# Kernel tuning notes

Hardware: AMD Instinct MI355X
Metric: run time of the kernel (lower is better)

## Reference

```python
import jax, jax.numpy as jnp
import numpy as np

B, S, H = 2, 2048, 1024
NQ, NKV, HD = 16, 4, 64
I, E, TOP_K = 3584, 8, 2
SLIDING_WINDOW = 512
EPS = 1e-5
MAX_WAVELENGTH = 10000.0


def setup_inputs() -> dict:
    key = jax.random.key(0)
    ks = jax.random.split(key, 10)
    p = lambda k, shape: jax.random.normal(k, shape, jnp.float32) * 0.02
    return {
        "decoder_sequence": jax.random.normal(ks[0], (B, S, H), jnp.float32),
        "norm1_scale": jnp.ones((H,), jnp.float32),
        "norm2_scale": jnp.ones((H,), jnp.float32),
        "wq": p(ks[1], (H, NQ, HD)),
        "wk": p(ks[2], (H, NKV, HD)),
        "wv": p(ks[3], (H, NKV, HD)),
        "wo": p(ks[4], (NQ, HD, H)),
        "w_router": p(ks[5], (H, E)),
        "w_gate": p(ks[6], (E, H, I)),
        "w_up": p(ks[7], (E, H, I)),
        "w_down": p(ks[8], (E, I, H)),
    }


def _rms_norm(x, scale, eps=EPS):
    x32 = x.astype(jnp.float32)
    var = jnp.mean(x32 * x32, axis=-1, keepdims=True)
    return (x32 * jax.lax.rsqrt(var + eps) * scale).astype(x.dtype)


def _rope(x):
    # x: [B, S, n_heads, head_dim]; keras-hub RotaryEmbedding (interleaved cos/sin,
    # half-split rotate then interleave via stack+reshape).
    seq_len, dim = x.shape[1], x.shape[3]
    inv_freq = 1.0 / (MAX_WAVELENGTH ** (jnp.arange(0, dim, 2, dtype=jnp.float32) / dim))
    freq = jnp.arange(seq_len, dtype=jnp.float32)[:, None] * inv_freq[None, :]  # [S, D/2]
    emb = jnp.stack((freq, freq), axis=-1).reshape(seq_len, dim)  # interleaved [S, D]
    cos = jnp.cos(emb)[None, :, None, :].astype(x.dtype)
    sin = jnp.sin(emb)[None, :, None, :].astype(x.dtype)
    x1, x2 = jnp.split(x, 2, axis=-1)
    half_rot = jnp.stack((-x2, x1), axis=-1).reshape(x.shape)
    return x * cos + half_rot * sin


def _forward(x, norm1_scale, norm2_scale, wq, wk, wv, wo, w_router, w_gate, w_up, w_down):
    b, s, h = x.shape
    # --- self attention block ---
    resid = x
    hs = _rms_norm(x, norm1_scale)
    q = jnp.einsum("bsh,hnd->bsnd", hs, wq)
    k = jnp.einsum("bsh,hnd->bsnd", hs, wk)
    v = jnp.einsum("bsh,hnd->bsnd", hs, wv)
    q, k = _rope(q), _rope(k)
    rep = q.shape[2] // k.shape[2]  # GQA group size
    k = jnp.repeat(k, rep, axis=2)
    v = jnp.repeat(v, rep, axis=2)
    scores = jnp.einsum("bqnd,bknd->bnqk", q, k) / jnp.sqrt(jnp.asarray(q.shape[-1], q.dtype))
    qi = jnp.arange(s)[:, None]
    ki = jnp.arange(s)[None, :]
    mask = (ki <= qi) & (ki > qi - SLIDING_WINDOW)  # causal + sliding window
    scores = jnp.where(mask[None, None], scores, jnp.asarray(-1e9, scores.dtype))
    probs = jax.nn.softmax(scores, axis=-1)
    attn = jnp.einsum("bnqk,bknd->bqnd", probs, v)
    x = jnp.einsum("bqnd,ndh->bqh", attn, wo) + resid
    # --- sparse MoE block ---
    resid = x
    hs = _rms_norm(x, norm2_scale)
    h2 = hs.reshape(-1, h)  # [T, H]
    router_logits = h2 @ w_router  # [T, E]
    rw = jax.nn.softmax(router_logits, axis=-1)
    topw, topi = jax.lax.top_k(rw, TOP_K)
    topw = topw / jnp.sum(topw, axis=-1, keepdims=True)
    t = h2.shape[0]
    combine = jnp.zeros((t, E), h2.dtype).at[jnp.arange(t)[:, None], topi].set(topw)
    out = jnp.zeros_like(h2)
    for e in range(E):  # fixed small expert loop; zero combine weight == not routed
        g = jax.nn.silu(h2 @ w_gate[e])
        u = h2 @ w_up[e]
        out = out + combine[:, e:e + 1] * ((u * g) @ w_down[e])
    decoder_output = out.reshape(b, s, h) + resid
    return decoder_output, router_logits


def reference(decoder_sequence, norm1_scale, norm2_scale, wq, wk, wv, wo,
              w_router, w_gate, w_up, w_down):
    return _forward(decoder_sequence, norm1_scale, norm2_scale, wq, wk, wv, wo,
                    w_router, w_gate, w_up, w_down)
```

## Files before the change

### kernel.cpp

```cpp
#include <hip/hip_runtime.h>
#include <hip/hip_bf16.h>
#include <cstdio>


typedef __bf16 bf16x8 __attribute__((ext_vector_type(8)));
typedef float f32x4 __attribute__((ext_vector_type(4)));

#define MFMA16(a, b, c) __builtin_amdgcn_mfma_f32_16x16x32_bf16((a), (b), (c), 0, 0, 0)
#define GL16(g, l)                                                             \
  __builtin_amdgcn_global_load_lds(                                            \
      (const __attribute__((address_space(1))) void*)(g),                      \
      (__attribute__((address_space(3))) void*)(l), 16, 0, 0)
#define WAIT_VM0() asm volatile("s_waitcnt vmcnt(0)" ::: "memory")
#define SETPRIO(n) __builtin_amdgcn_s_setprio(n)

__device__ __forceinline__ unsigned short f2bf(float f) {
  unsigned u = __builtin_bit_cast(unsigned, f);
  u += 0x7fffu + ((u >> 16) & 1u);
  return (unsigned short)(u >> 16);
}
__device__ __forceinline__ float bf2f(unsigned short h) {
  unsigned u = ((unsigned)h) << 16;
  return __builtin_bit_cast(float, u);
}
__device__ __forceinline__ int sw32(int row, int chunk) {
  return row * 32 + ((chunk ^ ((row >> 1) & 3)) * 8);
}

static constexpr size_t O_WQKVT_HI = 0;
static constexpr size_t SZ_WQKVT   = 1536UL * 1024 * 2;
static constexpr size_t O_WQKVT_LO = O_WQKVT_HI + SZ_WQKVT;
static constexpr size_t O_WOT_HI   = O_WQKVT_LO + SZ_WQKVT;
static constexpr size_t SZ_WOT     = 1024UL * 1024 * 2;
static constexpr size_t O_WOT_LO   = O_WOT_HI + SZ_WOT;
static constexpr size_t O_WGT      = O_WOT_LO + SZ_WOT;
static constexpr size_t SZ_WE      = 8UL * 3584 * 1024 * 2;
static constexpr size_t O_WUT      = O_WGT + SZ_WE;
static constexpr size_t O_WDT      = O_WUT + SZ_WE;
static constexpr size_t O_H2       = O_WDT + SZ_WE;
static constexpr size_t SZ_BF_TH   = 4096UL * 1024 * 2;
static constexpr size_t O_TOK      = O_H2 + SZ_BF_TH;
static constexpr size_t O_WGTL     = O_TOK + 8UL * 4096 * 4;
static constexpr size_t O_CNT      = O_WGTL + 8UL * 4096 * 4;
static constexpr size_t O_DYN      = O_CNT + 256;
static constexpr size_t O_HSHI  = O_DYN;
static constexpr size_t O_HSLO  = O_HSHI + SZ_BF_TH;
static constexpr size_t O_QKV   = O_HSLO + SZ_BF_TH;
static constexpr size_t O_QHI   = O_QKV + 4096UL * 1536 * 4;
static constexpr size_t O_QLO   = O_QHI + SZ_BF_TH;
static constexpr size_t O_KHI   = O_QLO + SZ_BF_TH;
static constexpr size_t SZ_BF_T256 = 4096UL * 256 * 2;
static constexpr size_t O_KLO   = O_KHI + SZ_BF_T256;
static constexpr size_t O_VTH   = O_KLO + SZ_BF_T256;
static constexpr size_t O_VTL   = O_VTH + SZ_BF_T256;
static constexpr size_t O_AHI   = O_VTL + SZ_BF_T256;
static constexpr size_t O_ALO   = O_AHI + SZ_BF_TH;
static constexpr size_t O_XATTN = O_ALO + SZ_BF_TH;
static constexpr size_t O_END   = O_XATTN + 4096UL * 1024 * 4;
static constexpr size_t O_ACT   = O_DYN;
static constexpr size_t WS_NEED = O_END;

__global__ void zero_cnt_kernel(int* c) {
  if (threadIdx.x < 8) c[threadIdx.x] = 0;
}

__global__ __launch_bounds__(256) void init_out_kernel(const float* __restrict__ x,
                                                       float* __restrict__ o) {
  const long i = (long)blockIdx.x * 256 + threadIdx.x;
  *(float4*)&o[i * 4] = *(const float4*)&x[i * 4];
}

__global__ __launch_bounds__(256) void rmsnorm_kernel(const float* __restrict__ x,
                                                      const float* __restrict__ scale,
                                                      unsigned short* __restrict__ hi,
                                                      unsigned short* __restrict__ lo) {
  const int t = blockIdx.x, tid = threadIdx.x;
  const float4 v = *(const float4*)&x[(long)t * 1024 + tid * 4];
  float ss = v.x * v.x + v.y * v.y + v.z * v.z + v.w * v.w;
#pragma unroll
  for (int off = 32; off >= 1; off >>= 1) ss += __shfl_down(ss, off);
  __shared__ float red[4];
  if ((tid & 63) == 0) red[tid >> 6] = ss;
  __syncthreads();
  const float r = rsqrtf((red[0] + red[1] + red[2] + red[3]) * (1.0f / 1024.0f) + 1e-5f);
  const float4 sc = *(const float4*)&scale[tid * 4];
  float o[4] = {v.x * r * sc.x, v.y * r * sc.y, v.z * r * sc.z, v.w * r * sc.w};
  ushort4 hh, ll;
  unsigned short* hp = (unsigned short*)&hh;
  unsigned short* lp = (unsigned short*)&ll;
#pragma unroll
  for (int i = 0; i < 4; ++i) {
    hp[i] = f2bf(o[i]);
    lp[i] = f2bf(o[i] - bf2f(hp[i]));
  }
  *(ushort4*)&hi[(long)t * 1024 + tid * 4] = hh;
  if (lo) *(ushort4*)&lo[(long)t * 1024 + tid * 4] = ll;
}

__global__ __launch_bounds__(256) void transpose_cvt(const float* __restrict__ src,
                                                     unsigned short* __restrict__ dst,
                                                     int R, int C, long zsrc, long zdst) {
  src += (long)blockIdx.z * zsrc;
  dst += (long)blockIdx.z * zdst;
  const int c0 = blockIdx.x * 64, r0 = blockIdx.y * 64, tid = threadIdx.x;
  __shared__ float tb[64][65];
#pragma unroll
  for (int p = 0; p < 4; ++p) {
    const int r = p * 16 + (tid >> 4), c = (tid & 15) * 4;
    const float4 v = *(const float4*)&src[(long)(r0 + r) * C + c0 + c];
    tb[c + 0][r] = v.x; tb[c + 1][r] = v.y; tb[c + 2][r] = v.z; tb[c + 3][r] = v.w;
  }
  __syncthreads();
  const int dr = tid >> 2, s0 = (tid & 3) * 16;
  __align__(16) unsigned short tmp[16];
#pragma unroll
  for (int i = 0; i < 16; ++i) tmp[i] = f2bf(tb[dr][s0 + i]);
  const long o = (long)(c0 + dr) * R + r0 + s0;
  *(uint4*)&dst[o] = *(const uint4*)&tmp[0];
  *(uint4*)&dst[o + 8] = *(const uint4*)&tmp[8];
}

__global__ __launch_bounds__(256) void transpose_cvt_split(const float* __restrict__ src,
                                                           unsigned short* __restrict__ dh,
                                                           unsigned short* __restrict__ dl,
                                                           int R, int C) {
  const int c0 = blockIdx.x * 64, r0 = blockIdx.y * 64, tid = threadIdx.x;
  __shared__ float tb[64][65];
#pragma unroll
  for (int p = 0; p < 4; ++p) {
    const int r = p * 16 + (tid >> 4), c = (tid & 15) * 4;
    const float4 v = *(const float4*)&src[(long)(r0 + r) * C + c0 + c];
    tb[c + 0][r] = v.x; tb[c + 1][r] = v.y; tb[c + 2][r] = v.z; tb[c + 3][r] = v.w;
  }
  __syncthreads();
  const int dr = tid >> 2, s0 = (tid & 3) * 16;
  __align__(16) unsigned short th[16], tl[16];
#pragma unroll
  for (int i = 0; i < 16; ++i) {
    const float f = tb[dr][s0 + i];
    th[i] = f2bf(f);
    tl[i] = f2bf(f - bf2f(th[i]));
  }
  const long o = (long)(c0 + dr) * R + r0 + s0;
  *(uint4*)&dh[o] = *(const uint4*)&th[0];
  *(uint4*)&dh[o + 8] = *(const uint4*)&th[8];
  *(uint4*)&dl[o] = *(const uint4*)&tl[0];
  *(uint4*)&dl[o + 8] = *(const uint4*)&tl[8];
}

__global__ __launch_bounds__(256) void gemm_split(const unsigned short* __restrict__ Ahi,
                                                  const unsigned short* __restrict__ Alo,
                                                  const unsigned short* __restrict__ Bhi,
                                                  const unsigned short* __restrict__ Blo,
                                                  const float* __restrict__ resid,
                                                  float* __restrict__ C,
                                                  int M, int N, int K) {
  __shared__ unsigned short Ash[2][4096], Asl[2][4096], Bsh[2][4096], Bsl[2][4096];
  const int tid = threadIdx.x, wid = tid >> 6, lane = tid & 63;
  const int m0 = blockIdx.y * 128, n0 = blockIdx.x * 128;
  const int wm = (wid >> 1) * 64, wn = (wid & 1) * 64;
  const int fr = lane & 15, fg = lane >> 4;
  const int srow = tid >> 2;
  const int scol = (((tid & 3) ^ ((tid >> 3) & 3))) * 8;
  const long aoff = (long)(m0 + srow) * K + scol;
  const long boff = (long)(n0 + srow) * K + scol;
  const long h64 = 64L * K;
  char* a0 = (char*)Ash[0] + wid * 1024; char* a1 = (char*)Ash[1] + wid * 1024;
  char* al0 = (char*)Asl[0] + wid * 1024; char* al1 = (char*)Asl[1] + wid * 1024;
  char* b0 = (char*)Bsh[0] + wid * 1024; char* b1 = (char*)Bsh[1] + wid * 1024;
  char* bl0 = (char*)Bsl[0] + wid * 1024; char* bl1 = (char*)Bsl[1] + wid * 1024;
#define GS_STAGE(koff, pah_, pal_, pbh_, pbl_)                                 \
  do {                                                                         \
    GL16(Ahi + aoff + (koff), (pah_));                                         \
    GL16(Ahi + aoff + h64 + (koff), (pah_) + 4096);                            \
    GL16(Alo + aoff + (koff), (pal_));                                         \
    GL16(Alo + aoff + h64 + (koff), (pal_) + 4096);                            \
    GL16(Bhi + boff + (koff), (pbh_));                                         \
    GL16(Bhi + boff + h64 + (koff), (pbh_) + 4096);                            \
    GL16(Blo + boff + (koff), (pbl_));                                         \
    GL16(Blo + boff + h64 + (koff), (pbl_) + 4096);                            \
  } while (0)
  f32x4 acc[4][4] = {};
  GS_STAGE(0, a0, al0, b0, bl0);
  WAIT_VM0();
  __syncthreads();
  int cur = 0;
  for (int k0 = 0; k0 < K; k0 += 32) {
    const int kn = k0 + 32;
    if (kn < K) {
      if (cur) GS_STAGE(kn, a0, al0, b0, bl0);
      else     GS_STAGE(kn, a1, al1, b1, bl1);
    }
    const unsigned short* As_ = Ash[cur];
    const unsigned short* Al_ = Asl[cur];
    const unsigned short* Bs_ = Bsh[cur];
    const unsigned short* Bl_ = Bsl[cur];
    bf16x8 ah[4], al[4], bh[4], bl[4];
#pragma unroll
    for (int i = 0; i < 4; ++i) {
      const int oA = sw32(wm + i * 16 + fr, fg);
      const int oB = sw32(wn + i * 16 + fr, fg);
      ah[i] = *(const bf16x8*)&As_[oA];
      al[i] = *(const bf16x8*)&Al_[oA];
      bh[i] = *(const bf16x8*)&Bs_[oB];
      bl[i] = *(const bf16x8*)&Bl_[oB];
    }
    SETPRIO(1);
#pragma unroll
    for (int i = 0; i < 4; ++i)
#pragma unroll
      for (int j = 0; j < 4; ++j) {
        acc[i][j] = MFMA16(al[i], bh[j], acc[i][j]);
        acc[i][j] = MFMA16(ah[i], bl[j], acc[i][j]);
        acc[i][j] = MFMA16(ah[i], bh[j], acc[i][j]);
      }
    SETPRIO(0);
    WAIT_VM0();
    __syncthreads();
    cur ^= 1;
  }
#undef GS_STAGE
  const int cr = fg * 4;
#pragma unroll
  for (int i = 0; i < 4; ++i)
#pragma unroll
    for (int j = 0; j < 4; ++j)
#pragma unroll
      for (int rr = 0; rr < 4; ++rr) {
        const int row = m0 + wm + i * 16 + cr + rr;
        const int col = n0 + wn + j * 16 + fr;
        float v = acc[i][j][rr];
        if (resid) v += resid[(long)row * N + col];
        C[(long)row * N + col] = v;
      }
}

__global__ __launch_bounds__(256) void rope_kernel(const float* __restrict__ qkv,
                                                   unsigned short* __restrict__ Qh,
                                                   unsigned short* __restrict__ Ql,
                                                   unsigned short* __restrict__ Kh,
                                                   unsigned short* __restrict__ Kl) {
  const int t = blockIdx.x, b = t >> 11, s = t & 2047;
  const float* src = qkv + (long)t * 1536;
  for (int task = threadIdx.x; task < 640; task += 256) {
    const int head = task >> 5, p = task & 31;
    const float* hp = src + head * 64;
    const float inv = (float)exp2(-(double)p * 0.4152410118609203);
    const float f = (float)s * inv;
    float sn, cs;
    sincosf(f, &sn, &cs);
    const float x0 = hp[2 * p], x1 = hp[2 * p + 1], xa = hp[p], xb = hp[32 + p];
    float o0 = x0 * cs - xb * sn;
    float o1 = x1 * cs + xa * sn;
    unsigned short *dh, *dl;
    long base;
    if (head < 16) {
      o0 *= 0.125f; o1 *= 0.125f;
      base = ((long)(b * 16 + head) * 2048 + s) * 64;
      dh = Qh; dl = Ql;
    } else {
      base = ((long)(b * 4 + (head - 16)) * 2048 + s) * 64;
      dh = Kh; dl = Kl;
    }
    unsigned short h0 = f2bf(o0);
    dh[base + 2 * p] = h0; dl[base + 2 * p] = f2bf(o0 - bf2f(h0));
    unsigned short h1 = f2bf(o1);
    dh[base + 2 * p + 1] = h1; dl[base + 2 * p + 1] = f2bf(o1 - bf2f(h1));
  }
}

__global__ __launch_bounds__(256) void vt_split_kernel(const float* __restrict__ qkv,
                                                       unsigned short* __restrict__ Vh,
                                                       unsigned short* __restrict__ Vl) {
  const int st = blockIdx.x * 64, g = blockIdx.y, b = blockIdx.z, tid = threadIdx.x;
  __shared__ float tb[64][65];
  const float* src = qkv + (long)(b * 2048 + st) * 1536 + 1280 + g * 64;
#pragma unroll
  for (int p = 0; p < 4; ++p) {
    const int r = p * 16 + (tid >> 4), c = (tid & 15) * 4;
    const float4 v = *(const float4*)&src[(long)r * 1536 + c];
    tb[c + 0][r] = v.x; tb[c + 1][r] = v.y; tb[c + 2][r] = v.z; tb[c + 3][r] = v.w;
  }
  __syncthreads();
  const int dr = tid >> 2, s0 = (tid & 3) * 16;
  __align__(16) unsigned short hh[16], ll[16];
#pragma unroll
  for (int i = 0; i < 16; ++i) {
    const float f = tb[dr][s0 + i];
    hh[i] = f2bf(f);
    ll[i] = f2bf(f - bf2f(hh[i]));
  }
  const long dst = ((long)(b * 4 + g) * 64 + dr) * 2048 + st + s0;
  *(uint4*)&Vh[dst] = *(const uint4*)&hh[0];
  *(uint4*)&Vh[dst + 8] = *(const uint4*)&hh[8];
  *(uint4*)&Vl[dst] = *(const uint4*)&ll[0];
  *(uint4*)&Vl[dst + 8] = *(const uint4*)&ll[8];
}

__global__ __launch_bounds__(256) void attn_kernel(const unsigned short* __restrict__ Qh,
                                                   const unsigned short* __restrict__ Ql,
                                                   const unsigned short* __restrict__ Kh,
                                                   const unsigned short* __restrict__ Kl,
                                                   const unsigned short* __restrict__ Vh,
                                                   const unsigned short* __restrict__ Vl,
                                                   unsigned short* __restrict__ Ohi,
                                                   unsigned short* __restrict__ Olo) {
  const int qt = blockIdx.x, h = blockIdx.y, b = blockIdx.z, g = h >> 2;
  const int q0 = qt * 64, tid = threadIdx.x, wid = tid >> 6, lane = tid & 63;
  const int fr = lane & 15, fg = lane >> 4;
  __shared__ unsigned short Ksh[2][2048], Ksl[2][2048];
  __shared__ unsigned short Vsh[2][2048], Vsl[2][2048];
  __shared__ unsigned short Ph[4][512], Pl[4][512];

  const long qoff = ((long)(b * 16 + h) * 2048 + q0 + wid * 16 + fr) * 64;
  bf16x8 qh[2], ql[2];
  qh[0] = *(const bf16x8*)&Qh[qoff + fg * 8];
  qh[1] = *(const bf16x8*)&Qh[qoff + 32 + fg * 8];
  ql[0] = *(const bf16x8*)&Ql[qoff + fg * 8];
  ql[1] = *(const bf16x8*)&Ql[qoff + 32 + fg * 8];

  f32x4 o[4] = {};
  float mrow[4], lrow[4];
#pragma unroll
  for (int rr = 0; rr < 4; ++rr) { mrow[rr] = -1e30f; lrow[rr] = 0.f; }

  const int jmin = (q0 >= 511) ? (q0 - 511) : 0;
  const int jt0 = jmin & ~31;
  const long kbase = ((long)(b * 4 + g) * 2048) * 64;
  const long vbase = ((long)(b * 4 + g) * 64) * 2048;
  const int srK = tid >> 3;
  const int scK = (((tid & 7) ^ (srK & 7))) * 8;
  const int srV = tid >> 2;
  const int scV = (((tid & 3) ^ ((srV >> 1) & 3))) * 8;
  char* kh0 = (char*)Ksh[0] + wid * 1024; char* kh1 = (char*)Ksh[1] + wid * 1024;
  char* kl0 = (char*)Ksl[0] + wid * 1024; char* kl1 = (char*)Ksl[1] + wid * 1024;
  char* vh0 = (char*)Vsh[0] + wid * 1024; char* vh1 = (char*)Vsh[1] + wid * 1024;
  char* vl0 = (char*)Vsl[0] + wid * 1024; char* vl1 = (char*)Vsl[1] + wid * 1024;
#define ATTN_STAGE(jt_, kh_, kl_, vh_, vl_)                                    \
  do {                                                                         \
    const long ko = kbase + (long)((jt_) + srK) * 64 + scK;                    \
    GL16(Kh + ko, (kh_));                                                      \
    GL16(Kl + ko, (kl_));                                                      \
    const long vo = vbase + (long)srV * 2048 + (jt_) + scV;                    \
    GL16(Vh + vo, (vh_));                                                      \
    GL16(Vl + vo, (vl_));                                                      \
  } while (0)

  ATTN_STAGE(jt0, kh0, kl0, vh0, vl0);
  WAIT_VM0();
  __syncthreads();
  int cur = 0;
  for (int jt = jt0; jt < q0 + 64; jt += 32) {
    const int jn = jt + 32;
    if (jn < q0 + 64) {
      if (cur) ATTN_STAGE(jn, kh0, kl0, vh0, vl0);
      else     ATTN_STAGE(jn, kh1, kl1, vh1, vl1);
    }
    const unsigned short* KH = Ksh[cur];
    const unsigned short* KL = Ksl[cur];
    const unsigned short* VH = Vsh[cur];
    const unsigned short* VL = Vsl[cur];

    f32x4 sf[2] = {};
#pragma unroll
    for (int cf = 0; cf < 2; ++cf)
#pragma unroll
      for (int dc = 0; dc < 2; ++dc) {
        const int row = cf * 16 + fr;
        const int off = row * 64 + (((dc * 4 + fg) ^ (row & 7)) * 8);
        const bf16x8 kh = *(const bf16x8*)&KH[off];
        const bf16x8 kl = *(const bf16x8*)&KL[off];
        sf[cf] = MFMA16(ql[dc], kh, sf[cf]);
        sf[cf] = MFMA16(qh[dc], kl, sf[cf]);
        sf[cf] = MFMA16(qh[dc], kh, sf[cf]);
      }

    float sv[2][4];
#pragma unroll
    for (int cf = 0; cf < 2; ++cf) {
      const int j = jt + cf * 16 + fr;
#pragma unroll
      for (int rr = 0; rr < 4; ++rr) {
        const int q = q0 + wid * 16 + fg * 4 + rr;
        const bool ok = (j <= q) && (j >= q - 511);
        sv[cf][rr] = ok ? sf[cf][rr] : -1e30f;
      }
    }
    float scl_[4];
#pragma unroll
    for (int rr = 0; rr < 4; ++rr) {
      float mx = fmaxf(sv[0][rr], sv[1][rr]);
      mx = fmaxf(mx, __shfl_xor(mx, 1));
      mx = fmaxf(mx, __shfl_xor(mx, 2));
      mx = fmaxf(mx, __shfl_xor(mx, 4));
      mx = fmaxf(mx, __shfl_xor(mx, 8));
      const float mn = fmaxf(mrow[rr], mx);
      scl_[rr] = __expf(mrow[rr] - mn);
      mrow[rr] = mn;
    }
    float ps[2][4], rs[4] = {0.f, 0.f, 0.f, 0.f};
#pragma unroll
    for (int cf = 0; cf < 2; ++cf)
#pragma unroll
      for (int rr = 0; rr < 4; ++rr) {
        const float p = (sv[cf][rr] > -1e29f) ? __expf(sv[cf][rr] - mrow[rr]) : 0.f;
        ps[cf][rr] = p;
        rs[rr] += p;
      }
#pragma unroll
    for (int rr = 0; rr < 4; ++rr) {
      float r = rs[rr];
      r += __shfl_xor(r, 1);
      r += __shfl_xor(r, 2);
      r += __shfl_xor(r, 4);
      r += __shfl_xor(r, 8);
      lrow[rr] = lrow[rr] * scl_[rr] + r;
      o[0][rr] *= scl_[rr]; o[1][rr] *= scl_[rr];
      o[2][rr] *= scl_[rr]; o[3][rr] *= scl_[rr];
    }
#pragma unroll
    for (int cf = 0; cf < 2; ++cf)
#pragma unroll
      for (int rr = 0; rr < 4; ++rr) {
        const int q = fg * 4 + rr, k = cf * 16 + fr;
        const int idx = q * 32 + (((k >> 3) ^ ((q >> 1) & 3)) * 8) + (k & 7);
        const unsigned short hb = f2bf(ps[cf][rr]);
        Ph[wid][idx] = hb;
        Pl[wid][idx] = f2bf(ps[cf][rr] - bf2f(hb));
      }
    const int pro = sw32(fr, fg);
    const bf16x8 pah = *(const bf16x8*)&Ph[wid][pro];
    const bf16x8 pal = *(const bf16x8*)&Pl[wid][pro];
#pragma unroll
    for (int df = 0; df < 4; ++df) {
      const int vo = sw32(df * 16 + fr, fg);
      const bf16x8 vh = *(const bf16x8*)&VH[vo];
      const bf16x8 vl = *(const bf16x8*)&VL[vo];
      o[df] = MFMA16(pal, vh, o[df]);
      o[df] = MFMA16(pah, vl, o[df]);
      o[df] = MFMA16(pah, vh, o[df]);
    }
    WAIT_VM0();
    __syncthreads();
    cur ^= 1;
  }
#undef ATTN_STAGE
#pragma unroll
  for (int df = 0; df < 4; ++df)
#pragma unroll
    for (int rr = 0; rr < 4; ++rr) {
      const int q = q0 + wid * 16 + fg * 4 + rr;
      const float v = o[df][rr] / lrow[rr];
      const long oi = ((long)(b * 2048 + q)) * 1024 + h * 64 + df * 16 + fr;
      const unsigned short hb = f2bf(v);
      Ohi[oi] = hb;
      Olo[oi] = f2bf(v - bf2f(hb));
    }
}

__global__ __launch_bounds__(256) void router_kernel(const float* __restrict__ xattn,
                                                     const float* __restrict__ scale,
                                                     const float* __restrict__ wr,
                                                     float* __restrict__ logits,
                                                     int* __restrict__ tok,
                                                     float* __restrict__ wgt,
                                                     int* __restrict__ cnt) {
  const int t = blockIdx.x, tid = threadIdx.x;
  const float4 v = *(const float4*)&xattn[(long)t * 1024 + tid * 4];
  float ss = v.x * v.x + v.y * v.y + v.z * v.z + v.w * v.w;
#pragma unroll
  for (int off = 32; off >= 1; off >>= 1) ss += __shfl_down(ss, off);
  __shared__ float red[4];
  __shared__ float redE[4][8];
  __shared__ float lg[8];
  if ((tid & 63) == 0) red[tid >> 6] = ss;
  __syncthreads();
  const float r = rsqrtf((red[0] + red[1] + red[2] + red[3]) * (1.0f / 1024.0f) + 1e-5f);
  const float4 sc = *(const float4*)&scale[tid * 4];
  const float hv[4] = {v.x * r * sc.x, v.y * r * sc.y, v.z * r * sc.z, v.w * r * sc.w};
  float part[8];
#pragma unroll
  for (int e = 0; e < 8; ++e) part[e] = 0.f;
#pragma unroll
  for (int i = 0; i < 4; ++i) {
    const float* w = &wr[(long)(tid * 4 + i) * 8];
#pragma unroll
    for (int e = 0; e < 8; ++e) part[e] = fmaf(hv[i], w[e], part[e]);
  }
#pragma unroll
  for (int off = 32; off >= 1; off >>= 1)
#pragma unroll
    for (int e = 0; e < 8; ++e) part[e] += __shfl_down(part[e], off);
  if ((tid & 63) == 0)
#pragma unroll
    for (int e = 0; e < 8; ++e) redE[tid >> 6][e] = part[e];
  __syncthreads();
  if (tid < 8) {
    const float l8 = redE[0][tid] + redE[1][tid] + redE[2][tid] + redE[3][tid];
    lg[tid] = l8;
    logits[(long)t * 8 + tid] = l8;
  }
  __syncthreads();
  if (tid == 0) {
    float mx = lg[0];
#pragma unroll
    for (int e = 1; e < 8; ++e) mx = fmaxf(mx, lg[e]);
    float p[8];
#pragma unroll
    for (int e = 0; e < 8; ++e) p[e] = __expf(lg[e] - mx);
    int i1 = 0;
#pragma unroll
    for (int e = 1; e < 8; ++e) if (p[e] > p[i1]) i1 = e;
    int i2 = (i1 == 0) ? 1 : 0;
#pragma unroll
    for (int e = 0; e < 8; ++e) if (e != i2 && e != i1 && p[e] > p[i2]) i2 = e;
    const float wsum = p[i1] + p[i2];
    const float w1 = p[i1] / wsum, w2 = p[i2] / wsum;
    const int pos1 = atomicAdd(&cnt[i1], 1);
    tok[i1 * 4096 + pos1] = t; wgt[i1 * 4096 + pos1] = w1;
    const int pos2 = atomicAdd(&cnt[i2], 1);
    tok[i2 * 4096 + pos2] = t; wgt[i2 * 4096 + pos2] = w2;
  }
}

__global__ __launch_bounds__(256) void gateup_kernel(const unsigned short* __restrict__ H2,
                                                     const unsigned short* __restrict__ WG,
                                                     const unsigned short* __restrict__ WU,
                                                     const int* __restrict__ tok,
                                                     const int* __restrict__ cnt,
                                                     unsigned short* __restrict__ act) {
  const int e = blockIdx.z;
  const int cn = cnt[e];
  const int m0 = blockIdx.y * 128;
  if (m0 >= cn) return;
  int padoff = 0;
  for (int i = 0; i < e; ++i) padoff += (cnt[i] + 127) & ~127;
  const int n0 = blockIdx.x * 128;
  __shared__ unsigned short As[2][4096], Bg[2][4096], Bu[2][4096];
  const int tid = threadIdx.x, wid = tid >> 6, lane = tid & 63;
  const int wm = (wid >> 1) * 64, wn = (wid & 1) * 64;
  const int fr = lane & 15, fg = lane >> 4;
  const int srow = tid >> 2;
  const int scol = (((tid & 3) ^ ((tid >> 3) & 3))) * 8;
  const int lr1 = m0 + srow, lr2 = lr1 + 64;
  const int tok1 = (lr1 < cn) ? tok[e * 4096 + lr1] : 0;
  const int tok2 = (lr2 < cn) ? tok[e * 4096 + lr2] : 0;
  const unsigned short* ga1 = H2 + (long)tok1 * 1024 + scol;
  const unsigned short* ga2 = H2 + (long)tok2 * 1024 + scol;
  const unsigned short* gb = WG + (long)e * 3584 * 1024 + (long)(n0 + srow) * 1024 + scol;
  const unsigned short* gu = WU + (long)e * 3584 * 1024 + (long)(n0 + srow) * 1024 + scol;
  char* a0 = (char*)As[0] + wid * 1024; char* a1 = (char*)As[1] + wid * 1024;
  char* g0 = (char*)Bg[0] + wid * 1024; char* g1 = (char*)Bg[1] + wid * 1024;
  char* u0 = (char*)Bu[0] + wid * 1024; char* u1 = (char*)Bu[1] + wid * 1024;
#define GU_STAGE(koff, pa_, pg_, pu_)                                          \
  do {                                                                         \
    GL16(ga1 + (koff), (pa_));                                                 \
    GL16(ga2 + (koff), (pa_) + 4096);                                          \
    GL16(gb + (koff), (pg_));                                                  \
    GL16(gb + 64L * 1024 + (koff), (pg_) + 4096);                              \
    GL16(gu + (koff), (pu_));                                                  \
    GL16(gu + 64L * 1024 + (koff), (pu_) + 4096);                              \
  } while (0)
  f32x4 ag[4][4] = {}, au[4][4] = {};
  GU_STAGE(0, a0, g0, u0);
  WAIT_VM0();
  __syncthreads();
  int cur = 0;
  for (int k0 = 0; k0 < 1024; k0 += 32) {
    const int kn = k0 + 32;
    if (kn < 1024) {
      if (cur) GU_STAGE(kn, a0, g0, u0);
      else     GU_STAGE(kn, a1, g1, u1);
    }
    const unsigned short* As_ = As[cur];
    const unsigned short* Bg_ = Bg[cur];
    const unsigned short* Bu_ = Bu[cur];
    bf16x8 af[4], bgf[4], buf_[4];
#pragma unroll
    for (int i = 0; i < 4; ++i) {
      const int oA = sw32(wm + i * 16 + fr, fg);
      const int oB = sw32(wn + i * 16 + fr, fg);
      af[i] = *(const bf16x8*)&As_[oA];
      bgf[i] = *(const bf16x8*)&Bg_[oB];
      buf_[i] = *(const bf16x8*)&Bu_[oB];
    }
    SETPRIO(1);
#pragma unroll
    for (int i = 0; i < 4; ++i)
#pragma unroll
      for (int j = 0; j < 4; ++j) {
        ag[i][j] = MFMA16(af[i], bgf[j], ag[i][j]);
        au[i][j] = MFMA16(af[i], buf_[j], au[i][j]);
      }
    SETPRIO(0);
    WAIT_VM0();
    __syncthreads();
    cur ^= 1;
  }
#undef GU_STAGE
  const int cr = fg * 4;
#pragma unroll
  for (int i = 0; i < 4; ++i)
#pragma unroll
    for (int j = 0; j < 4; ++j)
#pragma unroll
      for (int rr = 0; rr < 4; ++rr) {
        const int row = wm + i * 16 + cr + rr;
        const int col = n0 + wn + j * 16 + fr;
        const float gv = ag[i][j][rr];
        const float sg = gv / (1.f + __expf(-gv));
        act[(long)(padoff + m0 + row) * 3584 + col] = f2bf(sg * au[i][j][rr]);
      }
}

__global__ __launch_bounds__(256) void down_kernel(const unsigned short* __restrict__ act,
                                                   const unsigned short* __restrict__ WD,
                                                   const int* __restrict__ tok,
                                                   const float* __restrict__ wgt,
                                                   const int* __restrict__ cnt,
                                                   float* __restrict__ out) {
  const int e = blockIdx.z;
  const int cn = cnt[e];
  const int m0 = blockIdx.y * 128;
  if (m0 >= cn) return;
  int padoff = 0;
  for (int i = 0; i < e; ++i) padoff += (cnt[i] + 127) & ~127;
  const int n0 = blockIdx.x * 128;
  __shared__ unsigned short As[2][4096], Bs[2][4096];
  const int tid = threadIdx.x, wid = tid >> 6, lane = tid & 63;
  const int wm = (wid >> 1) * 64, wn = (wid & 1) * 64;
  const int fr = lane & 15, fg = lane >> 4;
  const int srow = tid >> 2;
  const int scol = (((tid & 3) ^ ((tid >> 3) & 3))) * 8;
  const unsigned short* ga = act + (long)(padoff + m0 + srow) * 3584 + scol;
  const unsigned short* gb = WD + (long)e * 1024 * 3584 + (long)(n0 + srow) * 3584 + scol;
  char* a0 = (char*)As[0] + wid * 1024; char* a1 = (char*)As[1] + wid * 1024;
  char* b0 = (char*)Bs[0] + wid * 1024; char* b1 = (char*)Bs[1] + wid * 1024;
#define DN_STAGE(koff, pa_, pb_)                                               \
  do {                                                                         \
    GL16(ga + (koff), (pa_));                                                  \
    GL16(ga + 64L * 3584 + (koff), (pa_) + 4096);                              \
    GL16(gb + (koff), (pb_));                                                  \
    GL16(gb + 64L * 3584 + (koff), (pb_) + 4096);                              \
  } while (0)
  f32x4 acc[4][4] = {};
  DN_STAGE(0, a0, b0);
  WAIT_VM0();
  __syncthreads();
  int cur = 0;
  for (int k0 = 0; k0 < 3584; k0 += 32) {
    const int kn = k0 + 32;
    if (kn < 3584) {
      if (cur) DN_STAGE(kn, a0, b0);
      else     DN_STAGE(kn, a1, b1);
    }
    const unsigned short* As_ = As[cur];
    const unsigned short* Bs_ = Bs[cur];
    bf16x8 af[4], bf_[4];
#pragma unroll
    for (int i = 0; i < 4; ++i) {
      const int oA = sw32(wm + i * 16 + fr, fg);
      const int oB = sw32(wn + i * 16 + fr, fg);
      af[i] = *(const bf16x8*)&As_[oA];
      bf_[i] = *(const bf16x8*)&Bs_[oB];
    }
    SETPRIO(1);
#pragma unroll
    for (int i = 0; i < 4; ++i)
#pragma unroll
      for (int j = 0; j < 4; ++j)
        acc[i][j] = MFMA16(af[i], bf_[j], acc[i][j]);
    SETPRIO(0);
    WAIT_VM0();
    __syncthreads();
    cur ^= 1;
  }
#undef DN_STAGE
  const int cr = fg * 4;
#pragma unroll
  for (int i = 0; i < 4; ++i)
#pragma unroll
    for (int rr = 0; rr < 4; ++rr) {
      const int lrow = m0 + wm + i * 16 + cr + rr;
      if (lrow < cn) {
        const int tk = tok[e * 4096 + lrow];
        const float w = wgt[e * 4096 + lrow];
#pragma unroll
        for (int j = 0; j < 4; ++j)
          atomicAdd(&out[(long)tk * 1024 + n0 + wn + j * 16 + fr], w * acc[i][j][rr]);
      }
    }
}

extern "C" void kernel_launch(void* const* d_in, const int* in_sizes, int n_in,
                              void* d_out, int out_size, void* d_ws, size_t ws_size,
                              hipStream_t stream) {
  (void)in_sizes; (void)n_in; (void)out_size;
  if (ws_size < WS_NEED) {
    fprintf(stderr, "kernel_launch: ws too small: %zu < %zu\n", ws_size, (size_t)WS_NEED);
  }
  const float* x    = (const float*)d_in[0];
  const float* n1s  = (const float*)d_in[1];
  const float* n2s  = (const float*)d_in[2];
  const float* wq   = (const float*)d_in[3];
  const float* wk   = (const float*)d_in[4];
  const float* wv   = (const float*)d_in[5];
  const float* wo   = (const float*)d_in[6];
  const float* wrt  = (const float*)d_in[7];
  const float* wg   = (const float*)d_in[8];
  const float* wu   = (const float*)d_in[9];
  const float* wd   = (const float*)d_in[10];
  float* out = (float*)d_out;
  char* W = (char*)d_ws;

  unsigned short* WQH = (unsigned short*)(W + O_WQKVT_HI);
  unsigned short* WQL = (unsigned short*)(W + O_WQKVT_LO);
  unsigned short* WOH = (unsigned short*)(W + O_WOT_HI);
  unsigned short* WOL = (unsigned short*)(W + O_WOT_LO);
  unsigned short* WGT = (unsigned short*)(W + O_WGT);
  unsigned short* WUT = (unsigned short*)(W + O_WUT);
  unsigned short* WDT = (unsigned short*)(W + O_WDT);
  unsigned short* H2  = (unsigned short*)(W + O_H2);
  int* TOK    = (int*)(W + O_TOK);
  float* WGTL = (float*)(W + O_WGTL);
  int* CNT    = (int*)(W + O_CNT);
  unsigned short* HSH = (unsigned short*)(W + O_HSHI);
  unsigned short* HSL = (unsigned short*)(W + O_HSLO);
  float* QKV = (float*)(W + O_QKV);
  unsigned short* QHI = (unsigned short*)(W + O_QHI);
  unsigned short* QLO = (unsigned short*)(W + O_QLO);
  unsigned short* KHI = (unsigned short*)(W + O_KHI);
  unsigned short* KLO = (unsigned short*)(W + O_KLO);
  unsigned short* VTH = (unsigned short*)(W + O_VTH);
  unsigned short* VTL = (unsigned short*)(W + O_VTL);
  unsigned short* AHI = (unsigned short*)(W + O_AHI);
  unsigned short* ALO = (unsigned short*)(W + O_ALO);
  float* XATTN = (float*)(W + O_XATTN);
  unsigned short* ACT = (unsigned short*)(W + O_ACT);

  zero_cnt_kernel<<<1, 64, 0, stream>>>(CNT);
  rmsnorm_kernel<<<4096, 256, 0, stream>>>(x, n1s, HSH, HSL);
  transpose_cvt_split<<<dim3(16, 16, 1), 256, 0, stream>>>(wq, WQH, WQL, 1024, 1024);
  transpose_cvt_split<<<dim3(4, 16, 1), 256, 0, stream>>>(wk, WQH + 1024L * 1024, WQL + 1024L * 1024, 1024, 256);
  transpose_cvt_split<<<dim3(4, 16, 1), 256, 0, stream>>>(wv, WQH + 1280L * 1024, WQL + 1280L * 1024, 1024, 256);
  transpose_cvt_split<<<dim3(16, 16, 1), 256, 0, stream>>>(wo, WOH, WOL, 1024, 1024);
  transpose_cvt<<<dim3(56, 16, 8), 256, 0, stream>>>(wg, WGT, 1024, 3584, 1024L * 3584, 3584L * 1024);
  transpose_cvt<<<dim3(56, 16, 8), 256, 0, stream>>>(wu, WUT, 1024, 3584, 1024L * 3584, 3584L * 1024);
  transpose_cvt<<<dim3(16, 56, 8), 256, 0, stream>>>(wd, WDT, 3584, 1024, 3584L * 1024, 1024L * 3584);
  gemm_split<<<dim3(12, 32, 1), 256, 0, stream>>>(HSH, HSL, WQH, WQL, nullptr, QKV, 4096, 1536, 1024);
  rope_kernel<<<4096, 256, 0, stream>>>(QKV, QHI, QLO, KHI, KLO);
  vt_split_kernel<<<dim3(32, 4, 2), 256, 0, stream>>>(QKV, VTH, VTL);
  attn_kernel<<<dim3(32, 16, 2), 256, 0, stream>>>(QHI, QLO, KHI, KLO, VTH, VTL, AHI, ALO);
  gemm_split<<<dim3(8, 32, 1), 256, 0, stream>>>(AHI, ALO, WOH, WOL, x, XATTN, 4096, 1024, 1024);
  rmsnorm_kernel<<<4096, 256, 0, stream>>>(XATTN, n2s, H2, nullptr);
  router_kernel<<<4096, 256, 0, stream>>>(XATTN, n2s, wrt, out + 4194304, TOK, WGTL, CNT);
  init_out_kernel<<<4096, 256, 0, stream>>>(XATTN, out);
  gateup_kernel<<<dim3(28, 32, 8), 256, 0, stream>>>(H2, WGT, WUT, TOK, CNT, ACT);
  down_kernel<<<dim3(8, 32, 8), 256, 0, stream>>>(ACT, WDT, TOK, WGTL, CNT, out);
}
```

Baseline: 755.8 us.

## Use 512-thread blocks and triple-buffered prefetch in MoE expert GEMMs

The gate/up and down expert GEMM kernels move from 256 to 512 threads per block, with 8 waves each computing a 64x32 sub-tile. Shared-memory staging goes from double to triple buffering, so loads run two k-steps ahead. A partial vmcnt wait plus barrier replaces the full drain each iteration. This aims to hide global-load latency and raise wave-level parallelism, at the cost of more LDS per block (72KB for gate/up) and fewer MFMAs per wave per LDS read.

```diff
diff --git a/kernel.cpp b/kernel.cpp
--- a/kernel.cpp
+++ b/kernel.cpp
@@ -13,6 +13,12 @@
       (__attribute__((address_space(3))) void*)(l), 16, 0, 0)
 #define WAIT_VM0() asm volatile("s_waitcnt vmcnt(0)" ::: "memory")
 #define SETPRIO(n) __builtin_amdgcn_s_setprio(n)
+#define PIPE_SYNC(n)                                                           \
+  do {                                                                         \
+    asm volatile("s_waitcnt vmcnt(" #n ")" ::: "memory");                      \
+    __builtin_amdgcn_s_barrier();                                              \
+    asm volatile("" ::: "memory");                                             \
+  } while (0)
 
 __device__ __forceinline__ unsigned short f2bf(float f) {
   unsigned u = __builtin_bit_cast(unsigned, f);
@@ -523,12 +529,12 @@
   }
 }
 
-__global__ __launch_bounds__(256) void gateup_kernel(const unsigned short* __restrict__ H2,
-                                                     const unsigned short* __restrict__ WG,
-                                                     const unsigned short* __restrict__ WU,
-                                                     const int* __restrict__ tok,
-                                                     const int* __restrict__ cnt,
-                                                     unsigned short* __restrict__ act) {
+__global__ __launch_bounds__(512, 4) void gateup_kernel(const unsigned short* __restrict__ H2,
+                                                        const unsigned short* __restrict__ WG,
+                                                        const unsigned short* __restrict__ WU,
+                                                        const int* __restrict__ tok,
+                                                        const int* __restrict__ cnt,
+                                                        unsigned short* __restrict__ act) {
   const int e = blockIdx.z;
   const int cn = cnt[e];
   const int m0 = blockIdx.y * 128;
@@ -536,73 +542,61 @@
   int padoff = 0;
   for (int i = 0; i < e; ++i) padoff += (cnt[i] + 127) & ~127;
   const int n0 = blockIdx.x * 128;
-  __shared__ unsigned short As[2][4096], Bg[2][4096], Bu[2][4096];
+  __shared__ unsigned short As[3][4096], Bg[3][4096], Bu[3][4096];
   const int tid = threadIdx.x, wid = tid >> 6, lane = tid & 63;
-  const int wm = (wid >> 1) * 64, wn = (wid & 1) * 64;
+  const int wm = (wid >> 2) * 64, wn = (wid & 3) * 32;
   const int fr = lane & 15, fg = lane >> 4;
   const int srow = tid >> 2;
   const int scol = (((tid & 3) ^ ((tid >> 3) & 3))) * 8;
-  const int lr1 = m0 + srow, lr2 = lr1 + 64;
-  const int tok1 = (lr1 < cn) ? tok[e * 4096 + lr1] : 0;
-  const int tok2 = (lr2 < cn) ? tok[e * 4096 + lr2] : 0;
-  const unsigned short* ga1 = H2 + (long)tok1 * 1024 + scol;
-  const unsigned short* ga2 = H2 + (long)tok2 * 1024 + scol;
+  const int lr = m0 + srow;
+  const int tkr = (lr < cn) ? tok[e * 4096 + lr] : 0;
+  const unsigned short* ga = H2 + (long)tkr * 1024 + scol;
   const unsigned short* gb = WG + (long)e * 3584 * 1024 + (long)(n0 + srow) * 1024 + scol;
   const unsigned short* gu = WU + (long)e * 3584 * 1024 + (long)(n0 + srow) * 1024 + scol;
-  char* a0 = (char*)As[0] + wid * 1024; char* a1 = (char*)As[1] + wid * 1024;
-  char* g0 = (char*)Bg[0] + wid * 1024; char* g1 = (char*)Bg[1] + wid * 1024;
-  char* u0 = (char*)Bu[0] + wid * 1024; char* u1 = (char*)Bu[1] + wid * 1024;
-#define GU_STAGE(koff, pa_, pg_, pu_)                                          \
+#define GU_STAGE(s, b)                                                         \
   do {                                                                         \
-    GL16(ga1 + (koff), (pa_));                                                 \
-    GL16(ga2 + (koff), (pa_) + 4096);                                          \
-    GL16(gb + (koff), (pg_));                                                  \
-    GL16(gb + 64L * 1024 + (koff), (pg_) + 4096);                              \
-    GL16(gu + (koff), (pu_));                                                  \
-    GL16(gu + 64L * 1024 + (koff), (pu_) + 4096);                              \
+    const int ko = (s) * 32;                                                   \
+    GL16(ga + ko, (char*)As[b] + wid * 1024);                                  \
+    GL16(gb + ko, (char*)Bg[b] + wid * 1024);                                  \
+    GL16(gu + ko, (char*)Bu[b] + wid * 1024);                                  \
   } while (0)
-  f32x4 ag[4][4] = {}, au[4][4] = {};
-  GU_STAGE(0, a0, g0, u0);
-  WAIT_VM0();
-  __syncthreads();
-  int cur = 0;
-  for (int k0 = 0; k0 < 1024; k0 += 32) {
-    const int kn = k0 + 32;
-    if (kn < 1024) {
-      if (cur) GU_STAGE(kn, a0, g0, u0);
-      else     GU_STAGE(kn, a1, g1, u1);
-    }
-    const unsigned short* As_ = As[cur];
-    const unsigned short* Bg_ = Bg[cur];
-    const unsigned short* Bu_ = Bu[cur];
-    bf16x8 af[4], bgf[4], buf_[4];
-#pragma unroll
-    for (int i = 0; i < 4; ++i) {
-      const int oA = sw32(wm + i * 16 + fr, fg);
-      const int oB = sw32(wn + i * 16 + fr, fg);
-      af[i] = *(const bf16x8*)&As_[oA];
-      bgf[i] = *(const bf16x8*)&Bg_[oB];
-      buf_[i] = *(const bf16x8*)&Bu_[oB];
+  f32x4 ag[4][2] = {}, au[4][2] = {};
+  GU_STAGE(0, 0);
+  GU_STAGE(1, 1);
+  PIPE_SYNC(3);
+  for (int t = 0; t < 32; ++t) {
+    const int cb = t % 3;
+    if (t + 2 < 32) GU_STAGE(t + 2, (t + 2) % 3);
+    const unsigned short* As_ = As[cb];
+    const unsigned short* Bg_ = Bg[cb];
+    const unsigned short* Bu_ = Bu[cb];
+    bf16x8 af[4], bgf[2], buf_[2];
+#pragma unroll
+    for (int i = 0; i < 4; ++i) af[i] = *(const bf16x8*)&As_[sw32(wm + i * 16 + fr, fg)];
+#pragma unroll
+    for (int j = 0; j < 2; ++j) {
+      const int oB = sw32(wn + j * 16 + fr, fg);
+      bgf[j] = *(const bf16x8*)&Bg_[oB];
+      buf_[j] = *(const bf16x8*)&Bu_[oB];
     }
     SETPRIO(1);
 #pragma unroll
     for (int i = 0; i < 4; ++i)
 #pragma unroll
-      for (int j = 0; j < 4; ++j) {
+      for (int j = 0; j < 2; ++j) {
         ag[i][j] = MFMA16(af[i], bgf[j], ag[i][j]);
         au[i][j] = MFMA16(af[i], buf_[j], au[i][j]);
       }
     SETPRIO(0);
-    WAIT_VM0();
-    __syncthreads();
-    cur ^= 1;
+    if (t + 2 < 32) PIPE_SYNC(3);
+    else if (t + 1 < 32) PIPE_SYNC(0);
   }
 #undef GU_STAGE
   const int cr = fg * 4;
 #pragma unroll
   for (int i = 0; i < 4; ++i)
 #pragma unroll
-    for (int j = 0; j < 4; ++j)
+    for (int j = 0; j < 2; ++j)
 #pragma unroll
       for (int rr = 0; rr < 4; ++rr) {
         const int row = wm + i * 16 + cr + rr;
@@ -613,12 +607,12 @@
       }
 }
 
-__global__ __launch_bounds__(256) void down_kernel(const unsigned short* __restrict__ act,
-                                                   const unsigned short* __restrict__ WD,
-                                                   const int* __restrict__ tok,
-                                                   const float* __restrict__ wgt,
-                                                   const int* __restrict__ cnt,
-                                                   float* __restrict__ out) {
+__global__ __launch_bounds__(512, 4) void down_kernel(const unsigned short* __restrict__ act,
+                                                      const unsigned short* __restrict__ WD,
+                                                      const int* __restrict__ tok,
+                                                      const float* __restrict__ wgt,
+                                                      const int* __restrict__ cnt,
+                                                      float* __restrict__ out) {
   const int e = blockIdx.z;
   const int cn = cnt[e];
   const int m0 = blockIdx.y * 128;
@@ -626,54 +620,43 @@
   int padoff = 0;
   for (int i = 0; i < e; ++i) padoff += (cnt[i] + 127) & ~127;
   const int n0 = blockIdx.x * 128;
-  __shared__ unsigned short As[2][4096], Bs[2][4096];
+  __shared__ unsigned short As[3][4096], Bs[3][4096];
   const int tid = threadIdx.x, wid = tid >> 6, lane = tid & 63;
-  const int wm = (wid >> 1) * 64, wn = (wid & 1) * 64;
+  const int wm = (wid >> 2) * 64, wn = (wid & 3) * 32;
   const int fr = lane & 15, fg = lane >> 4;
   const int srow = tid >> 2;
   const int scol = (((tid & 3) ^ ((tid >> 3) & 3))) * 8;
   const unsigned short* ga = act + (long)(padoff + m0 + srow) * 3584 + scol;
   const unsigned short* gb = WD + (long)e * 1024 * 3584 + (long)(n0 + srow) * 3584 + scol;
-  char* a0 = (char*)As[0] + wid * 1024; char* a1 = (char*)As[1] + wid * 1024;
-  char* b0 = (char*)Bs[0] + wid * 1024; char* b1 = (char*)Bs[1] + wid * 1024;
-#define DN_STAGE(koff, pa_, pb_)                                               \
+#define DN_STAGE(s, b)                                                         \
   do {                                                                         \
-    GL16(ga + (koff), (pa_));                                                  \
-    GL16(ga + 64L * 3584 + (koff), (pa_) + 4096);                              \
-    GL16(gb + (koff), (pb_));                                                  \
-    GL16(gb + 64L * 3584 + (koff), (pb_) + 4096);                              \
+    const int ko = (s) * 32;                                                   \
+    GL16(ga + ko, (char*)As[b] + wid * 1024);                                  \
+    GL16(gb + ko, (char*)Bs[b] + wid * 1024);                                  \
   } while (0)
-  f32x4 acc[4][4] = {};
-  DN_STAGE(0, a0, b0);
-  WAIT_VM0();
-  __syncthreads();
-  int cur = 0;
-  for (int k0 = 0; k0 < 3584; k0 += 32) {
-    const int kn = k0 + 32;
-    if (kn < 3584) {
-      if (cur) DN_STAGE(kn, a0, b0);
-      else     DN_STAGE(kn, a1, b1);
-    }
-    const unsigned short* As_ = As[cur];
-    const unsigned short* Bs_ = Bs[cur];
-    bf16x8 af[4], bf_[4];
-#pragma unroll
-    for (int i = 0; i < 4; ++i) {
-      const int oA = sw32(wm + i * 16 + fr, fg);
-      const int oB = sw32(wn + i * 16 + fr, fg);
-      af[i] = *(const bf16x8*)&As_[oA];
-      bf_[i] = *(const bf16x8*)&Bs_[oB];
-    }
+  f32x4 acc[4][2] = {};
+  DN_STAGE(0, 0);
+  DN_STAGE(1, 1);
+  PIPE_SYNC(2);
+  for (int t = 0; t < 112; ++t) {
+    const int cb = t % 3;
+    if (t + 2 < 112) DN_STAGE(t + 2, (t + 2) % 3);
+    const unsigned short* As_ = As[cb];
+    const unsigned short* Bs_ = Bs[cb];
+    bf16x8 af[4], bf_[2];
+#pragma unroll
+    for (int i = 0; i < 4; ++i) af[i] = *(const bf16x8*)&As_[sw32(wm + i * 16 + fr, fg)];
+#pragma unroll
+    for (int j = 0; j < 2; ++j) bf_[j] = *(const bf16x8*)&Bs_[sw32(wn + j * 16 + fr, fg)];
     SETPRIO(1);
 #pragma unroll
     for (int i = 0; i < 4; ++i)
 #pragma unroll
-      for (int j = 0; j < 4; ++j)
+      for (int j = 0; j < 2; ++j)
         acc[i][j] = MFMA16(af[i], bf_[j], acc[i][j]);
     SETPRIO(0);
-    WAIT_VM0();
-    __syncthreads();
-    cur ^= 1;
+    if (t + 2 < 112) PIPE_SYNC(2);
+    else if (t + 1 < 112) PIPE_SYNC(0);
   }
 #undef DN_STAGE
   const int cr = fg * 4;
@@ -686,7 +669,7 @@
         const int tk = tok[e * 4096 + lrow];
         const float w = wgt[e * 4096 + lrow];
 #pragma unroll
-        for (int j = 0; j < 4; ++j)
+        for (int j = 0; j < 2; ++j)
           atomicAdd(&out[(long)tk * 1024 + n0 + wn + j * 16 + fr], w * acc[i][j][rr]);
       }
     }
@@ -755,6 +738,6 @@
   rmsnorm_kernel<<<4096, 256, 0, stream>>>(XATTN, n2s, H2, nullptr);
   router_kernel<<<4096, 256, 0, stream>>>(XATTN, n2s, wrt, out + 4194304, TOK, WGTL, CNT);
   init_out_kernel<<<4096, 256, 0, stream>>>(XATTN, out);
-  gateup_kernel<<<dim3(28, 32, 8), 256, 0, stream>>>(H2, WGT, WUT, TOK, CNT, ACT);
-  down_kernel<<<dim3(8, 32, 8), 256, 0, stream>>>(ACT, WDT, TOK, WGTL, CNT, out);
-}
+  gateup_kernel<<<dim3(28, 32, 8), 512, 0, stream>>>(H2, WGT, WUT, TOK, CNT, ACT);
+  down_kernel<<<dim3(8, 32, 8), 512, 0, stream>>>(ACT, WDT, TOK, WGTL, CNT, out);
+}
```

Result: faster. 712.5 us (-5.7%).
